# Kernel optimization log

Measured on AMD Instinct MI355X. Metric: run time of the kernel, lower is better.

Reference implementation:

```python
import jax, jax.numpy as jnp
import numpy as np

M, N, D, H, E = 100000, 50000, 128, 2, 1000000
NEG_SLOPE = 0.2  # standard GAT LeakyReLU slope


def setup_inputs() -> dict:
    key = jax.random.key(0)
    ks = jax.random.split(key, 14)
    inp = {
        "u_prev": jax.random.normal(ks[0], (M, D), jnp.float32),
        "i_prev": jax.random.normal(ks[1], (N, D), jnp.float32),
        "w_user": jax.random.normal(ks[2], (D, D), jnp.float32) * 0.05,
        "b_user": jax.random.normal(ks[3], (D,), jnp.float32) * 0.05,
        "w_item": jax.random.normal(ks[4], (D, D), jnp.float32) * 0.05,
        "b_item": jax.random.normal(ks[5], (D,), jnp.float32) * 0.05,
        "a_u_src": jax.random.normal(ks[6], (H, D), jnp.float32) * 0.1,
        "a_u_dst": jax.random.normal(ks[7], (H, D), jnp.float32) * 0.1,
        "a_i_src": jax.random.normal(ks[8], (H, D), jnp.float32) * 0.1,
        "a_i_dst": jax.random.normal(ks[9], (H, D), jnp.float32) * 0.1,
        "u2i_row": jax.random.randint(ks[10], (E,), 0, M, jnp.int32),
        "u2i_col": jax.random.randint(ks[11], (E,), 0, N, jnp.int32),
        "i2u_row": jax.random.randint(ks[12], (E,), 0, N, jnp.int32),
        "i2u_col": jax.random.randint(ks[13], (E,), 0, M, jnp.int32),
    }
    return inp


def _segment_softmax(logits, seg, num_segments):
    # neighborhood softmax: normalize per adjacency row
    mx = jax.ops.segment_max(logits, seg, num_segments=num_segments)
    e = jnp.exp(logits - mx[seg])
    s = jax.ops.segment_sum(e, seg, num_segments=num_segments)
    return e / s[seg]


def _attend(row, col, h_src, h_dst, a_src, a_dst, num_src):
    hs = h_src[row]  # (E, D) gather of source-node features
    hd = h_dst[col]  # (E, D) gather of dest-node features
    head_outs = []
    for h in range(a_src.shape[0]):  # small fixed head count
        logits = jax.nn.leaky_relu(hs @ a_src[h] + hd @ a_dst[h], NEG_SLOPE)  # (E,)
        att = _segment_softmax(logits, row, num_src)                         # (E,)
        # sparse att @ h_dst == row-segment sum of att-weighted neighbor features
        head_outs.append(jax.ops.segment_sum(att[:, None] * hd, row, num_segments=num_src))
    out = sum(head_outs) / len(head_outs)  # reduce_att = mean over heads
    return jax.nn.elu(out)                  # self.nonlinear


def reference(u_prev, i_prev, w_user, b_user, w_item, b_item,
              a_u_src, a_u_dst, a_i_src, a_i_dst,
              u2i_row, u2i_col, i2u_row, i2u_col):
    u = u_prev @ w_user + b_user  # (M, D)
    i = i_prev @ w_item + b_item  # (N, D)
    u_next = _attend(u2i_row, u2i_col, u, i, a_u_src, a_u_dst, M)
    i_next = _attend(i2u_row, i2u_col, i, u, a_i_src, a_i_dst, N)
    return (u_next, i_next)
```

## Files before the change

kernel.cpp:

```cpp
#include <hip/hip_runtime.h>
#include <cstdint>
#include <cstddef>

#define D 128
#define NEG_SLOPE 0.2f
#define CAP 64

__device__ __forceinline__ float lrelu(float x) { return x > 0.0f ? x : NEG_SLOPE * x; }
__device__ __forceinline__ float elu_f(float x) { return x > 0.0f ? x : expm1f(x); }
__device__ __forceinline__ unsigned short f2bf(float f) {
    unsigned u = __float_as_uint(f);
    return (unsigned short)((u + 0x7fffu + ((u >> 16) & 1u)) >> 16);
}

typedef __attribute__((ext_vector_type(8))) short bf16x8;
typedef __attribute__((ext_vector_type(4))) float f32x4;

__global__ __launch_bounds__(256) void prep_w_zero(
    const float* __restrict__ Wu, const float* __restrict__ Wi,
    unsigned short* __restrict__ WswU, unsigned short* __restrict__ WswI,
    int* __restrict__ cntA, int M, int* __restrict__ cntB, int N)
{
    int b = (int)blockIdx.x;
    if (b < 16) {
        bool di = b >= 8;
        const float* W = di ? Wi : Wu;
        unsigned short* Wsw = di ? WswI : WswU;
        int c = (b & 7) * 256 + (int)threadIdx.x;
        int n = c >> 4, s = c & 15;
        const float* src = W + (size_t)(s * 8) * D + n;
        unsigned t0 = ((unsigned)f2bf(src[0 * D])) | ((unsigned)f2bf(src[1 * D]) << 16);
        unsigned t1 = ((unsigned)f2bf(src[2 * D])) | ((unsigned)f2bf(src[3 * D]) << 16);
        unsigned t2 = ((unsigned)f2bf(src[4 * D])) | ((unsigned)f2bf(src[5 * D]) << 16);
        unsigned t3 = ((unsigned)f2bf(src[6 * D])) | ((unsigned)f2bf(src[7 * D]) << 16);
        *(uint4*)((char*)Wsw + n * 256 + ((s * 16) ^ ((n & 7) << 4))) = make_uint4(t0, t1, t2, t3);
        return;
    }
    int nA4 = M >> 2, nB4 = N >> 2;
    int total4 = nA4 + nB4;
    int stride = ((int)gridDim.x - 16) * 256;
    int4 z = make_int4(0, 0, 0, 0);
    for (int j = (b - 16) * 256 + (int)threadIdx.x; j < total4; j += stride) {
        if (j < nA4) ((int4*)cntA)[j] = z;
        else ((int4*)cntB)[j - nA4] = z;
    }
}

struct GemmDir {
    const float* A; const unsigned short* Wsw; const float* bias;
    const float* v0; const float* v1; const float* v2; const float* v3;
    unsigned short* Cb;
    float4* att; int R;
};

__global__ __launch_bounds__(512) void gemm_att(GemmDir g0, int nb0, GemmDir g1)
{
    int gb = blockIdx.x;
    const bool second = gb >= nb0;
    GemmDir g = second ? g1 : g0;
    const int bid = second ? (gb - nb0) : gb;

    __shared__ unsigned short Wl[128 * 128];

    const int tid = threadIdx.x;
    const int wave = tid >> 6;
    const int lane = tid & 63;
    const int lm = lane & 15;
    const int lg = lane >> 4;

    {
        const uint4* wsrc = (const uint4*)g.Wsw;
#pragma unroll
        for (int q = 0; q < 4; ++q) {
            int c = tid + q * 512;
            *(uint4*)((char*)Wl + (size_t)c * 16) = wsrc[c];
        }
    }
    __syncthreads();

    const int xr = (lm & 7) << 4;
    const float* vs[4] = { g.v0, g.v1, g.v2, g.v3 };
    const int colb = lg << 2;

#pragma unroll
    for (int t = 0; t < 2; ++t) {
        const int rowbase = bid * 256 + t * 128 + wave * 16;
        int ar = rowbase + lm;
        if (ar > g.R - 1) ar = g.R - 1;
        const float* Arow = g.A + (size_t)ar * D;

        f32x4 acc[8];
#pragma unroll
        for (int nt = 0; nt < 8; ++nt) { acc[nt][0] = 0.f; acc[nt][1] = 0.f; acc[nt][2] = 0.f; acc[nt][3] = 0.f; }

#pragma unroll
        for (int ks = 0; ks < 4; ++ks) {
            const float4 a0 = *(const float4*)(Arow + ks * 32 + lg * 8);
            const float4 a1 = *(const float4*)(Arow + ks * 32 + lg * 8 + 4);
            bf16x8 af;
            af[0] = (short)f2bf(a0.x); af[1] = (short)f2bf(a0.y);
            af[2] = (short)f2bf(a0.z); af[3] = (short)f2bf(a0.w);
            af[4] = (short)f2bf(a1.x); af[5] = (short)f2bf(a1.y);
            af[6] = (short)f2bf(a1.z); af[7] = (short)f2bf(a1.w);
            const int slot = ks * 4 + lg;
            const char* bbase = (const char*)Wl + lm * 256 + ((slot * 16) ^ xr);
#pragma unroll
            for (int nt = 0; nt < 8; ++nt) {
                bf16x8 wf = *(const bf16x8*)(bbase + nt * 4096);
                acc[nt] = __builtin_amdgcn_mfma_f32_16x16x32_bf16(wf, af, acc[nt], 0, 0, 0);
            }
        }

        const int row = rowbase + lm;
        const bool valid = row < g.R;

#pragma unroll
        for (int nt = 0; nt < 8; ++nt) {
            float4 bv = *(const float4*)(g.bias + nt * 16 + colb);
            acc[nt][0] += bv.x; acc[nt][1] += bv.y; acc[nt][2] += bv.z; acc[nt][3] += bv.w;
        }
        if (valid) {
#pragma unroll
            for (int nt = 0; nt < 8; ++nt) {
                ushort4 s = { f2bf(acc[nt][0]), f2bf(acc[nt][1]), f2bf(acc[nt][2]), f2bf(acc[nt][3]) };
                *(ushort4*)(g.Cb + (size_t)row * D + nt * 16 + colb) = s;
            }
        }

        float p[4];
#pragma unroll
        for (int h = 0; h < 4; ++h) {
            float s = 0.f;
#pragma unroll
            for (int nt = 0; nt < 8; ++nt) {
                float4 vh = *(const float4*)(vs[h] + nt * 16 + colb);
                s += acc[nt][0] * vh.x + acc[nt][1] * vh.y + acc[nt][2] * vh.z + acc[nt][3] * vh.w;
            }
            p[h] = s;
        }
#pragma unroll
        for (int h = 0; h < 4; ++h) {
            p[h] += __shfl_xor(p[h], 16, 64);
            p[h] += __shfl_xor(p[h], 32, 64);
        }
        if (lg == 0 && valid) g.att[row] = make_float4(p[0], p[1], p[2], p[3]);
    }
}

__global__ __launch_bounds__(256) void scatter_fill(
    const int* __restrict__ rowA, const int* __restrict__ colA,
    int* __restrict__ cntA, int* __restrict__ slotA, int EA, int chunkA,
    const int* __restrict__ rowB, const int* __restrict__ colB,
    int* __restrict__ cntB, int* __restrict__ slotB, int EB, int chunkB)
{
    int half = gridDim.x >> 1;
    bool dB = (int)blockIdx.x >= half;
    int b = dB ? (int)blockIdx.x - half : (int)blockIdx.x;
    const int* row = dB ? rowB : rowA;
    const int* col = dB ? colB : colA;
    int* cnt  = dB ? cntB : cntA;
    int* slot = dB ? slotB : slotA;
    int E = dB ? EB : EA;
    int chunk = dB ? chunkB : chunkA;

    int part = b & 7;
    int idx  = b >> 3;
    int nper = half >> 3;
    int lo = part * chunk, hi = lo + chunk;

    for (int i = idx * 256 + (int)threadIdx.x; i < E; i += nper * 256) {
        int r = row[i];
        if (r >= lo && r < hi) {
            int pos = atomicAdd(&cnt[r], 1);
            if (pos < CAP) slot[(size_t)r * CAP + pos] = col[i];
        }
    }
}

__device__ __forceinline__ void aggregate_row(
    const int* __restrict__ cnt, const int* __restrict__ slot,
    const char* __restrict__ satt, const char* __restrict__ datt,
    const unsigned short* __restrict__ featb,
    float* __restrict__ out, int seg, int lane)
{
    int deg = cnt[seg];
    deg = deg > CAP ? CAP : deg;
    float2 sa = *(const float2*)(satt + (size_t)seg * 16);
    float accx = 0.0f, accy = 0.0f;
    if (deg > 0) {
        int myc = 0;
        float e0 = 0.0f, e1 = 0.0f;
        if (lane < deg) {
            myc = slot[(size_t)seg * CAP + lane];
            float2 da = *(const float2*)(datt + (size_t)myc * 16);
            e0 = __expf(lrelu(sa.x + da.x));
            e1 = __expf(lrelu(sa.y + da.y));
        }
        float s0 = e0, s1 = e1;
#pragma unroll
        for (int o = 32; o > 0; o >>= 1) {
            s0 += __shfl_xor(s0, o, 64);
            s1 += __shfl_xor(s1, o, 64);
        }
        float myw = e0 * (0.5f / s0) + e1 * (0.5f / s1);
        float a0x = 0.f, a0y = 0.f, a1x = 0.f, a1y = 0.f,
              a2x = 0.f, a2y = 0.f, a3x = 0.f, a3y = 0.f;
        int j = 0;
        for (; j + 4 <= deg; j += 4) {
            int c0 = __shfl(myc, j, 64), c1 = __shfl(myc, j + 1, 64);
            int c2 = __shfl(myc, j + 2, 64), c3 = __shfl(myc, j + 3, 64);
            float w0 = __shfl(myw, j, 64), w1 = __shfl(myw, j + 1, 64);
            float w2 = __shfl(myw, j + 2, 64), w3 = __shfl(myw, j + 3, 64);
            unsigned f0 = *(const unsigned*)(featb + (size_t)c0 * D + 2 * lane);
            unsigned f1 = *(const unsigned*)(featb + (size_t)c1 * D + 2 * lane);
            unsigned f2 = *(const unsigned*)(featb + (size_t)c2 * D + 2 * lane);
            unsigned f3 = *(const unsigned*)(featb + (size_t)c3 * D + 2 * lane);
            a0x += w0 * __uint_as_float(f0 << 16); a0y += w0 * __uint_as_float(f0 & 0xffff0000u);
            a1x += w1 * __uint_as_float(f1 << 16); a1y += w1 * __uint_as_float(f1 & 0xffff0000u);
            a2x += w2 * __uint_as_float(f2 << 16); a2y += w2 * __uint_as_float(f2 & 0xffff0000u);
            a3x += w3 * __uint_as_float(f3 << 16); a3y += w3 * __uint_as_float(f3 & 0xffff0000u);
        }
        for (; j < deg; ++j) {
            int c0 = __shfl(myc, j, 64);
            float w0 = __shfl(myw, j, 64);
            unsigned f0 = *(const unsigned*)(featb + (size_t)c0 * D + 2 * lane);
            a0x += w0 * __uint_as_float(f0 << 16); a0y += w0 * __uint_as_float(f0 & 0xffff0000u);
        }
        accx = (a0x + a1x) + (a2x + a3x);
        accy = (a0y + a1y) + (a2y + a3y);
    }
    *(float2*)(out + (size_t)seg * D + 2 * lane) = make_float2(elu_f(accx), elu_f(accy));
}

__global__ __launch_bounds__(256) void aggregate_both(
    const int* cntA, const int* slotA, const char* sattA, const char* dattA,
    const unsigned short* featA, float* outA, int SA, int nbA,
    const int* cntB, const int* slotB, const char* sattB, const char* dattB,
    const unsigned short* featB, float* outB, int SB)
{
    int lane = threadIdx.x & 63;
    if (blockIdx.x < (unsigned)nbA) {
        int seg = blockIdx.x * 4 + (threadIdx.x >> 6);
        if (seg < SA) aggregate_row(cntA, slotA, sattA, dattA, featA, outA, seg, lane);
    } else {
        int seg = (blockIdx.x - nbA) * 4 + (threadIdx.x >> 6);
        if (seg < SB) aggregate_row(cntB, slotB, sattB, dattB, featB, outB, seg, lane);
    }
}

extern "C" void kernel_launch(void* const* d_in, const int* in_sizes, int n_in,
                              void* d_out, int out_size, void* d_ws, size_t ws_size,
                              hipStream_t stream)
{
    const float* u_prev  = (const float*)d_in[0];
    const float* i_prev  = (const float*)d_in[1];
    const float* w_user  = (const float*)d_in[2];
    const float* b_user  = (const float*)d_in[3];
    const float* w_item  = (const float*)d_in[4];
    const float* b_item  = (const float*)d_in[5];
    const float* a_u_src = (const float*)d_in[6];
    const float* a_u_dst = (const float*)d_in[7];
    const float* a_i_src = (const float*)d_in[8];
    const float* a_i_dst = (const float*)d_in[9];
    const int* u2i_row = (const int*)d_in[10];
    const int* u2i_col = (const int*)d_in[11];
    const int* i2u_row = (const int*)d_in[12];
    const int* i2u_col = (const int*)d_in[13];

    const int M = in_sizes[0] / D;
    const int N = in_sizes[1] / D;
    const int EA = in_sizes[10];
    const int EB = in_sizes[12];

    char* ws = (char*)d_ws;
    size_t off = 0;
    auto carve = [&](size_t bytes) -> char* {
        char* p = ws + off;
        off += (bytes + 255) & ~(size_t)255;
        return p;
    };
    unsigned short* u_featb = (unsigned short*)carve((size_t)M * D * 2);
    unsigned short* i_featb = (unsigned short*)carve((size_t)N * D * 2);
    float4* u_att   = (float4*)carve((size_t)M * 16);
    float4* i_att   = (float4*)carve((size_t)N * 16);
    int*    cntA    = (int*)carve((size_t)M * 4);
    int*    cntB    = (int*)carve((size_t)N * 4);
    int*    slotA   = (int*)carve((size_t)M * CAP * 4);
    int*    slotB   = (int*)carve((size_t)N * CAP * 4);
    unsigned short* wswU = (unsigned short*)carve((size_t)D * D * 2);
    unsigned short* wswI = (unsigned short*)carve((size_t)D * D * 2);
    (void)ws_size; (void)n_in; (void)out_size;

    prep_w_zero<<<16 + 160, 256, 0, stream>>>(w_user, w_item, wswU, wswI,
                                              cntA, M, cntB, N);

    GemmDir gu = { u_prev, wswU, b_user, a_u_src, a_u_src + D, a_i_dst, a_i_dst + D, u_featb, u_att, M };
    GemmDir gi = { i_prev, wswI, b_item, a_u_dst, a_u_dst + D, a_i_src, a_i_src + D, i_featb, i_att, N };
    int nbGu = (M + 255) / 256, nbGi = (N + 255) / 256;
    gemm_att<<<nbGu + nbGi, 512, 0, stream>>>(gu, nbGu, gi);

    int chunkA = (M + 7) / 8, chunkB = (N + 7) / 8;
    scatter_fill<<<2048, 256, 0, stream>>>(u2i_row, u2i_col, cntA, slotA, EA, chunkA,
                                           i2u_row, i2u_col, cntB, slotB, EB, chunkB);

    float* out_u = (float*)d_out;
    float* out_i = out_u + (size_t)M * D;
    int nbAggA = (M + 3) / 4, nbAggB = (N + 3) / 4;
    aggregate_both<<<nbAggA + nbAggB, 256, 0, stream>>>(
        cntA, slotA, (const char*)u_att, (const char*)i_att, i_featb, out_u, M, nbAggA,
        cntB, slotB, (const char*)i_att + 8, (const char*)u_att + 8, u_featb, out_i, N);
}
```

Baseline: 396.2 us.

## Fuse GEMM and edge scatter into one launch; use readlane broadcasts

Merges the projection GEMM kernel and the CSR scatter-fill kernel into a single interleaved grid, even blocks scattering edges and odd blocks computing GEMM tiles. This removes a launch boundary and lets the memory-bound atomic scatter overlap with the GEMM. In aggregation, shuffle-based broadcasts of neighbor index and weight are replaced by scalar readlane, avoiding cross-lane permute instructions. The fused kernel allocates 32KB of LDS per block even for scatter blocks, which may limit occupancy.

```diff
diff --git a/kernel.cpp b/kernel.cpp
--- a/kernel.cpp
+++ b/kernel.cpp
@@ -53,16 +53,46 @@
     float4* att; int R;
 };
 
-__global__ __launch_bounds__(512) void gemm_att(GemmDir g0, int nb0, GemmDir g1)
-{
-    int gb = blockIdx.x;
+__global__ __launch_bounds__(512) void gemm_scatter(
+    GemmDir g0, int nb0, GemmDir g1, int nbG,
+    const int* __restrict__ rowA, const int* __restrict__ colA,
+    int* __restrict__ cntA, int* __restrict__ slotA, int EA, int chunkA,
+    const int* __restrict__ rowB, const int* __restrict__ colB,
+    int* __restrict__ cntB, int* __restrict__ slotB, int EB, int chunkB)
+{
+    __shared__ unsigned short Wl[128 * 128];
+    const int bidx = (int)blockIdx.x;
+    const int tid = threadIdx.x;
+
+    if (!(bidx & 1)) {
+        int s = bidx >> 1;
+        bool dB = s >= 512;
+        int b = dB ? s - 512 : s;
+        const int* row = dB ? rowB : rowA;
+        const int* col = dB ? colB : colA;
+        int* cnt  = dB ? cntB : cntA;
+        int* slot = dB ? slotB : slotA;
+        int E = dB ? EB : EA;
+        int chunk = dB ? chunkB : chunkA;
+        int part = b & 7;
+        int idx  = b >> 3;
+        int lo = part * chunk, hi = lo + chunk;
+        for (int i = idx * 512 + tid; i < E; i += 64 * 512) {
+            int r = row[i];
+            if (r >= lo && r < hi) {
+                int pos = atomicAdd(&cnt[r], 1);
+                if (pos < CAP) slot[(size_t)r * CAP + pos] = col[i];
+            }
+        }
+        return;
+    }
+
+    int gb = bidx >> 1;
+    if (gb >= nbG) return;
     const bool second = gb >= nb0;
     GemmDir g = second ? g1 : g0;
     const int bid = second ? (gb - nb0) : gb;
 
-    __shared__ unsigned short Wl[128 * 128];
-
-    const int tid = threadIdx.x;
     const int wave = tid >> 6;
     const int lane = tid & 63;
     const int lm = lane & 15;
@@ -144,36 +174,6 @@
             p[h] += __shfl_xor(p[h], 32, 64);
         }
         if (lg == 0 && valid) g.att[row] = make_float4(p[0], p[1], p[2], p[3]);
-    }
-}
-
-__global__ __launch_bounds__(256) void scatter_fill(
-    const int* __restrict__ rowA, const int* __restrict__ colA,
-    int* __restrict__ cntA, int* __restrict__ slotA, int EA, int chunkA,
-    const int* __restrict__ rowB, const int* __restrict__ colB,
-    int* __restrict__ cntB, int* __restrict__ slotB, int EB, int chunkB)
-{
-    int half = gridDim.x >> 1;
-    bool dB = (int)blockIdx.x >= half;
-    int b = dB ? (int)blockIdx.x - half : (int)blockIdx.x;
-    const int* row = dB ? rowB : rowA;
-    const int* col = dB ? colB : colA;
-    int* cnt  = dB ? cntB : cntA;
-    int* slot = dB ? slotB : slotA;
-    int E = dB ? EB : EA;
-    int chunk = dB ? chunkB : chunkA;
-
-    int part = b & 7;
-    int idx  = b >> 3;
-    int nper = half >> 3;
-    int lo = part * chunk, hi = lo + chunk;
-
-    for (int i = idx * 256 + (int)threadIdx.x; i < E; i += nper * 256) {
-        int r = row[i];
-        if (r >= lo && r < hi) {
-            int pos = atomicAdd(&cnt[r], 1);
-            if (pos < CAP) slot[(size_t)r * CAP + pos] = col[i];
-        }
     }
 }
 
@@ -203,14 +203,20 @@
             s1 += __shfl_xor(s1, o, 64);
         }
         float myw = e0 * (0.5f / s0) + e1 * (0.5f / s1);
+        unsigned mywu = __float_as_uint(myw);
+
         float a0x = 0.f, a0y = 0.f, a1x = 0.f, a1y = 0.f,
               a2x = 0.f, a2y = 0.f, a3x = 0.f, a3y = 0.f;
         int j = 0;
         for (; j + 4 <= deg; j += 4) {
-            int c0 = __shfl(myc, j, 64), c1 = __shfl(myc, j + 1, 64);
-            int c2 = __shfl(myc, j + 2, 64), c3 = __shfl(myc, j + 3, 64);
-            float w0 = __shfl(myw, j, 64), w1 = __shfl(myw, j + 1, 64);
-            float w2 = __shfl(myw, j + 2, 64), w3 = __shfl(myw, j + 3, 64);
+            int c0 = __builtin_amdgcn_readlane(myc, j);
+            int c1 = __builtin_amdgcn_readlane(myc, j + 1);
+            int c2 = __builtin_amdgcn_readlane(myc, j + 2);
+            int c3 = __builtin_amdgcn_readlane(myc, j + 3);
+            float w0 = __uint_as_float(__builtin_amdgcn_readlane(mywu, j));
+            float w1 = __uint_as_float(__builtin_amdgcn_readlane(mywu, j + 1));
+            float w2 = __uint_as_float(__builtin_amdgcn_readlane(mywu, j + 2));
+            float w3 = __uint_as_float(__builtin_amdgcn_readlane(mywu, j + 3));
             unsigned f0 = *(const unsigned*)(featb + (size_t)c0 * D + 2 * lane);
             unsigned f1 = *(const unsigned*)(featb + (size_t)c1 * D + 2 * lane);
             unsigned f2 = *(const unsigned*)(featb + (size_t)c2 * D + 2 * lane);
@@ -221,8 +227,8 @@
             a3x += w3 * __uint_as_float(f3 << 16); a3y += w3 * __uint_as_float(f3 & 0xffff0000u);
         }
         for (; j < deg; ++j) {
-            int c0 = __shfl(myc, j, 64);
-            float w0 = __shfl(myw, j, 64);
+            int c0 = __builtin_amdgcn_readlane(myc, j);
+            float w0 = __uint_as_float(__builtin_amdgcn_readlane(mywu, j));
             unsigned f0 = *(const unsigned*)(featb + (size_t)c0 * D + 2 * lane);
             a0x += w0 * __uint_as_float(f0 << 16); a0y += w0 * __uint_as_float(f0 & 0xffff0000u);
         }
@@ -297,11 +303,11 @@
     GemmDir gu = { u_prev, wswU, b_user, a_u_src, a_u_src + D, a_i_dst, a_i_dst + D, u_featb, u_att, M };
     GemmDir gi = { i_prev, wswI, b_item, a_u_dst, a_u_dst + D, a_i_src, a_i_src + D, i_featb, i_att, N };
     int nbGu = (M + 255) / 256, nbGi = (N + 255) / 256;
-    gemm_att<<<nbGu + nbGi, 512, 0, stream>>>(gu, nbGu, gi);
-
     int chunkA = (M + 7) / 8, chunkB = (N + 7) / 8;
-    scatter_fill<<<2048, 256, 0, stream>>>(u2i_row, u2i_col, cntA, slotA, EA, chunkA,
-                                           i2u_row, i2u_col, cntB, slotB, EB, chunkB);
+    gemm_scatter<<<2048, 512, 0, stream>>>(
+        gu, nbGu, gi, nbGu + nbGi,
+        u2i_row, u2i_col, cntA, slotA, EA, chunkA,
+        i2u_row, i2u_col, cntB, slotB, EB, chunkB);
 
     float* out_u = (float*)d_out;
     float* out_i = out_u + (size_t)M * D;
```

After: 459.0 us. 1.16x slower.
